# Kernel optimization log

Measured on AMD Instinct MI355X. Metric: run time of the kernel, lower is better.

The kernel has to match this reference:

```python
import jax, jax.numpy as jnp
import numpy as np

HIDDEN = 512
ANN = 512


def setup_inputs() -> dict:
    key = jax.random.key(0)
    k1, k2, k3, k4, k5, k6 = jax.random.split(key, 6)
    B, S = 32, 4096
    prev_hidden_state = jax.random.normal(k1, (B, HIDDEN), dtype=jnp.float32)
    annotations = jax.random.normal(k2, (B, S, ANN), dtype=jnp.float32)
    in_dim = HIDDEN + ANN
    # Kaiming-uniform-ish init like torch Linear
    lim1 = 1.0 / np.sqrt(in_dim)
    W1 = jax.random.uniform(k3, (in_dim, HIDDEN), dtype=jnp.float32, minval=-lim1, maxval=lim1)
    b1 = jax.random.uniform(k4, (HIDDEN,), dtype=jnp.float32, minval=-lim1, maxval=lim1)
    lim2 = 1.0 / np.sqrt(HIDDEN)
    W2 = jax.random.uniform(k5, (HIDDEN, 1), dtype=jnp.float32, minval=-lim2, maxval=lim2)
    b2 = jax.random.uniform(k6, (1,), dtype=jnp.float32, minval=-lim2, maxval=lim2)
    return {"prev_hidden_state": prev_hidden_state, "annotations": annotations,
            "W1": W1, "b1": b1, "W2": W2, "b2": b2}


def reference(prev_hidden_state, annotations, W1, b1, W2, b2):
    # Split W1 so we never materialize the [B,S,hidden+ann] concat:
    # concat([h_rep, ann]) @ W1 == h @ W1[:H] + ann @ W1[H:]
    W1_h, W1_a = W1[:HIDDEN], W1[HIDDEN:]
    # [B,1,H] + [B,S,H] -> [B,S,H]
    pre = prev_hidden_state @ W1_h  # [B,H]
    hidden = jnp.tanh(pre[:, None, :] + jnp.einsum('bsa,ah->bsh', annotations, W1_a) + b1)
    score = jnp.einsum('bsh,h->bs', hidden, W2[:, 0]) + b2[0]  # [B,S]
    alpha = jax.nn.softmax(score, axis=1)  # legacy F.softmax default dim=1
    # alpha.bmm(annotations): [B,1,S] @ [B,S,A] -> [B,1,A]
    context = jnp.einsum('bs,bsa->ba', alpha, annotations)[:, None, :]
    return context
```

## Files before the change

kernel.cpp:

```cpp
#include <hip/hip_runtime.h>

#define HID 512
#define SEQ 4096
#define NB 32
#define BS 64
#define NSB 8
#define CPB 8
#define CH2 1026

typedef __attribute__((ext_vector_type(8))) __bf16 bf16x8;
typedef __attribute__((ext_vector_type(16))) float f32x16;

__device__ __forceinline__ float tanh_fast(float v) {
    float e = __expf(2.f * v);
    return 1.f - __fdividef(2.f, e + 1.f);
}

__global__ void build_w1af(const float* __restrict__ W1,
                           unsigned short* __restrict__ w1af) {
    __shared__ float tile[64][65];
    int t = threadIdx.x;
    int lane = t & 63;
    int r4 = t >> 6;
    int k0 = blockIdx.x * 64;
    int h0 = blockIdx.y * 64;
#pragma unroll
    for (int i = 0; i < 16; ++i) {
        int r = i * 4 + r4;
        tile[r][lane] = W1[(size_t)(HID + k0 + r) * HID + h0 + lane];
    }
    __syncthreads();
#pragma unroll
    for (int i = 0; i < 16; ++i) {
        int hr = i * 4 + r4;
        int h = h0 + hr, k = k0 + lane;
        __bf16 bv = (__bf16)tile[lane][hr];
        int ht = h >> 5, hl = h & 31;
        int ks = k >> 4, g = (k >> 3) & 1, j = k & 7;
        size_t off = (((size_t)ht * 32 + ks) * 64 + g * 32 + hl) * 8 + j;
        w1af[off] = *(unsigned short*)&bv;
    }
}

__global__ void pre_partial(const float* __restrict__ prev,
                            const float* __restrict__ W1,
                            float* __restrict__ pre_part) {
    __shared__ float pl[128];
    int kc = blockIdx.x;
    int b  = blockIdx.y;
    int t  = threadIdx.x;
    if (t < 128) pl[t] = prev[b * HID + kc * 128 + t];
    __syncthreads();
    int h0 = 2 * t;
    float ax = 0.f, ay = 0.f;
    for (int k = 0; k < 128; ++k) {
        float pv = pl[k];
        float2 wv = *(const float2*)(W1 + (size_t)(kc * 128 + k) * HID + h0);
        ax += pv * wv.x;
        ay += pv * wv.y;
    }
    float* dst = pre_part + ((size_t)b * 4 + kc) * HID + h0;
    dst[0] = ax; dst[1] = ay;
}

__global__ __launch_bounds__(1024, 4)
void score_ctx(const float* __restrict__ ann,
               const unsigned short* __restrict__ w1af,
               const float* __restrict__ pre_part,
               const float* __restrict__ b1,
               const float* __restrict__ W2,
               float* __restrict__ cout) {
    __shared__ unsigned short annA[BS * 512];
    __shared__ unsigned short annB[BS * 512];
    __shared__ float pre_lds[512];
    __shared__ float w2_lds[512];
    __shared__ float red[16][64];
    __shared__ float p_lds[64];
    __shared__ float md[2];

    const int sb = blockIdx.x, b = blockIdx.y;
    const int t = threadIdx.x;
    const int wv = t >> 6;
    const int lane = t & 63;
    const int sl = lane & 31;
    const int g = lane >> 5;

    if (t < 512) {
        float pp = b1[t];
#pragma unroll
        for (int kc = 0; kc < 4; ++kc)
            pp += pre_part[((size_t)b * 4 + kc) * HID + t];
        pre_lds[t] = pp;
    } else {
        w2_lds[t - 512] = W2[t - 512];
    }

    const float* abase = ann + ((size_t)b * SEQ + (size_t)sb * (CPB * BS)) * 512;

    float4 sf[8];
    {
#pragma unroll
        for (int i = 0; i < 4; ++i) {
            int idx = t + i * 1024;
            const float4* src = (const float4*)(abase + (size_t)(idx >> 6) * 512 + (idx & 63) * 8);
            sf[2 * i] = src[0]; sf[2 * i + 1] = src[1];
        }
#pragma unroll
        for (int i = 0; i < 4; ++i) {
            int idx = t + i * 1024;
            int row = idx >> 6, k8 = (idx & 63) * 8;
            bf16x8 pk;
            pk[0] = (__bf16)sf[2*i].x;   pk[1] = (__bf16)sf[2*i].y;
            pk[2] = (__bf16)sf[2*i].z;   pk[3] = (__bf16)sf[2*i].w;
            pk[4] = (__bf16)sf[2*i+1].x; pk[5] = (__bf16)sf[2*i+1].y;
            pk[6] = (__bf16)sf[2*i+1].z; pk[7] = (__bf16)sf[2*i+1].w;
            unsigned boff = ((unsigned)(row * 512 + k8) * 2u) ^ ((unsigned)(row & 7) << 4);
            *(bf16x8*)((char*)annA + boff) = pk;
        }
    }
    __syncthreads();

    float m_run = -3.0e38f, d_run = 0.f, ctx = 0.f;
    const int col = t & 511, half = t >> 9;

    const unsigned short* wb = w1af + (size_t)wv * 16384 + (size_t)lane * 8;
    const unsigned be0 = (unsigned)(sl * 512 + g * 8) * 2u;
    const unsigned be1 = (unsigned)((32 + sl) * 512 + g * 8) * 2u;
    const unsigned swz = (unsigned)(sl & 7) << 4;

#pragma unroll 1
    for (int c = 0; c < CPB; ++c) {
        unsigned short* curb = (c & 1) ? annB : annA;
        unsigned short* nxtb = (c & 1) ? annA : annB;

        if (c < CPB - 1) {
            const float* ab = abase + (size_t)(c + 1) * BS * 512;
#pragma unroll
            for (int i = 0; i < 4; ++i) {
                int idx = t + i * 1024;
                const float4* src = (const float4*)(ab + (size_t)(idx >> 6) * 512 + (idx & 63) * 8);
                sf[2 * i] = src[0]; sf[2 * i + 1] = src[1];
            }
        }

        f32x16 acc0, acc1;
#pragma unroll
        for (int r = 0; r < 16; ++r) { acc0[r] = 0.f; acc1[r] = 0.f; }
#pragma unroll 2
        for (int ks = 0; ks < 32; ++ks) {
            bf16x8 a = *(const bf16x8*)(wb + ks * 512);
            bf16x8 bf0 = *(const bf16x8*)((const char*)curb + ((be0 + (unsigned)ks * 32u) ^ swz));
            bf16x8 bf1 = *(const bf16x8*)((const char*)curb + ((be1 + (unsigned)ks * 32u) ^ swz));
            acc0 = __builtin_amdgcn_mfma_f32_32x32x16_bf16(a, bf0, acc0, 0, 0, 0);
            acc1 = __builtin_amdgcn_mfma_f32_32x32x16_bf16(a, bf1, acc1, 0, 0, 0);
        }

        float sp0 = 0.f, sp1 = 0.f;
#pragma unroll
        for (int r = 0; r < 16; ++r) {
            int h = wv * 32 + (r & 3) + 8 * (r >> 2) + 4 * g;
            float pr = pre_lds[h], w2v = w2_lds[h];
            sp0 += w2v * tanh_fast(acc0[r] + pr);
            sp1 += w2v * tanh_fast(acc1[r] + pr);
        }
        sp0 += __shfl_xor(sp0, 32);
        sp1 += __shfl_xor(sp1, 32);
        if (lane < 32) { red[wv][lane] = sp0; red[wv][32 + lane] = sp1; }
        __syncthreads();

        if (wv == 0) {
            float sc = 0.f;
#pragma unroll
            for (int q = 0; q < 16; ++q) sc += red[q][lane];
            float m = sc;
#pragma unroll
            for (int off = 32; off; off >>= 1) m = fmaxf(m, __shfl_xor(m, off));
            float p = __expf(sc - m);
            float d = p;
#pragma unroll
            for (int off = 32; off; off >>= 1) d += __shfl_xor(d, off);
            p_lds[lane] = p;
            if (lane == 0) { md[0] = m; md[1] = d; }
        }
        __syncthreads();

        float m_c = md[0], d_c = md[1];
        float m_new = fmaxf(m_run, m_c);
        float sc_old = __expf(m_run - m_new);
        float sc_c = __expf(m_c - m_new);
        d_run = d_run * sc_old + d_c * sc_c;
        float na = 0.f;
        const char* cb8 = (const char*)curb;
#pragma unroll 8
        for (int s2 = 0; s2 < 32; ++s2) {
            int s = half * 32 + s2;
            unsigned boff = ((unsigned)(s * 512 + col) * 2u) ^ ((unsigned)(s & 7) << 4);
            unsigned short us = *(const unsigned short*)(cb8 + boff);
            na += p_lds[s] * __uint_as_float((unsigned)us << 16);
        }
        ctx = ctx * sc_old + na * sc_c;
        m_run = m_new;

        if (c < CPB - 1) {
            __syncthreads();
#pragma unroll
            for (int i = 0; i < 4; ++i) {
                int idx = t + i * 1024;
                int row = idx >> 6, k8 = (idx & 63) * 8;
                bf16x8 pk;
                pk[0] = (__bf16)sf[2*i].x;   pk[1] = (__bf16)sf[2*i].y;
                pk[2] = (__bf16)sf[2*i].z;   pk[3] = (__bf16)sf[2*i].w;
                pk[4] = (__bf16)sf[2*i+1].x; pk[5] = (__bf16)sf[2*i+1].y;
                pk[6] = (__bf16)sf[2*i+1].z; pk[7] = (__bf16)sf[2*i+1].w;
                unsigned boff = ((unsigned)(row * 512 + k8) * 2u) ^ ((unsigned)(row & 7) << 4);
                *(bf16x8*)((char*)nxtb + boff) = pk;
            }
            __syncthreads();
        }
    }

    float* cb = cout + ((size_t)b * NSB + sb) * CH2;
    cb[2 + half * 512 + col] = ctx;
    if (t == 0) { cb[0] = m_run; cb[1] = d_run; }
}

__global__ void finalize_ctx(const float* __restrict__ cout,
                             float* __restrict__ out) {
    int b = blockIdx.x, t = threadIdx.x;
    float ms[NSB];
    float M = -3.0e38f;
#pragma unroll
    for (int s = 0; s < NSB; ++s) {
        ms[s] = cout[((size_t)b * NSB + s) * CH2];
        M = fmaxf(M, ms[s]);
    }
    float D = 0.f, val = 0.f;
#pragma unroll
    for (int s = 0; s < NSB; ++s) {
        const float* cb = cout + ((size_t)b * NSB + s) * CH2;
        float e = __expf(ms[s] - M);
        D += e * cb[1];
        val += e * (cb[2 + t] + cb[2 + 512 + t]);
    }
    out[(size_t)b * 512 + t] = val / D;
}

extern "C" void kernel_launch(void* const* d_in, const int* in_sizes, int n_in,
                              void* d_out, int out_size, void* d_ws, size_t ws_size,
                              hipStream_t stream) {
    (void)in_sizes; (void)n_in; (void)out_size; (void)ws_size;
    const float* prev = (const float*)d_in[0];
    const float* ann  = (const float*)d_in[1];
    const float* W1   = (const float*)d_in[2];
    const float* b1   = (const float*)d_in[3];
    const float* W2   = (const float*)d_in[4];
    float* out = (float*)d_out;

    char* ws = (char*)d_ws;
    unsigned short* w1af = (unsigned short*)ws;
    float* pre_part = (float*)(ws + 524288);
    float* cout     = (float*)(ws + 524288 + 262144);

    build_w1af<<<dim3(8, 8), dim3(256), 0, stream>>>(W1, w1af);
    pre_partial<<<dim3(4, NB), dim3(256), 0, stream>>>(prev, W1, pre_part);
    score_ctx<<<dim3(NSB, NB), dim3(1024), 0, stream>>>(ann, w1af, pre_part, b1, W2, cout);
    finalize_ctx<<<dim3(NB), dim3(512), 0, stream>>>(cout, out);
}
```

Measured before the change: 151.6 us.

## Use 128-row chunks with 512 threads and 2x4 MFMA register tiles per wave

Chunk size doubles to 128 rows and the block shrinks to 8 waves. Each wave now computes a 64x128 output tile with eight MFMA accumulators, so each W1 fragment is reused across four B tiles. The double-buffered LDS with register prefetch is replaced by a single buffer that is loaded synchronously, which removes the overlap of global loads with compute. The context accumulation reads two bf16 values per 32-bit LDS load.

```diff
diff --git a/kernel.cpp b/kernel.cpp
--- a/kernel.cpp
+++ b/kernel.cpp
@@ -3,9 +3,9 @@
 #define HID 512
 #define SEQ 4096
 #define NB 32
-#define BS 64
+#define BS 128
 #define NSB 8
-#define CPB 8
+#define CPB 4
 #define CH2 1026
 
 typedef __attribute__((ext_vector_type(8))) __bf16 bf16x8;
@@ -63,19 +63,18 @@
     dst[0] = ax; dst[1] = ay;
 }
 
-__global__ __launch_bounds__(1024, 4)
+__global__ __launch_bounds__(512, 2)
 void score_ctx(const float* __restrict__ ann,
                const unsigned short* __restrict__ w1af,
                const float* __restrict__ pre_part,
                const float* __restrict__ b1,
                const float* __restrict__ W2,
                float* __restrict__ cout) {
-    __shared__ unsigned short annA[BS * 512];
-    __shared__ unsigned short annB[BS * 512];
+    __shared__ unsigned short ann_lds[BS * 512];
     __shared__ float pre_lds[512];
     __shared__ float w2_lds[512];
-    __shared__ float red[16][64];
-    __shared__ float p_lds[64];
+    __shared__ float red[8][BS];
+    __shared__ float p_lds[BS];
     __shared__ float md[2];
 
     const int sb = blockIdx.x, b = blockIdx.y;
@@ -85,142 +84,134 @@
     const int sl = lane & 31;
     const int g = lane >> 5;
 
-    if (t < 512) {
+    {
         float pp = b1[t];
 #pragma unroll
         for (int kc = 0; kc < 4; ++kc)
             pp += pre_part[((size_t)b * 4 + kc) * HID + t];
         pre_lds[t] = pp;
-    } else {
-        w2_lds[t - 512] = W2[t - 512];
-    }
-
-    const float* abase = ann + ((size_t)b * SEQ + (size_t)sb * (CPB * BS)) * 512;
-
-    float4 sf[8];
-    {
-#pragma unroll
-        for (int i = 0; i < 4; ++i) {
-            int idx = t + i * 1024;
-            const float4* src = (const float4*)(abase + (size_t)(idx >> 6) * 512 + (idx & 63) * 8);
-            sf[2 * i] = src[0]; sf[2 * i + 1] = src[1];
-        }
-#pragma unroll
-        for (int i = 0; i < 4; ++i) {
-            int idx = t + i * 1024;
-            int row = idx >> 6, k8 = (idx & 63) * 8;
-            bf16x8 pk;
-            pk[0] = (__bf16)sf[2*i].x;   pk[1] = (__bf16)sf[2*i].y;
-            pk[2] = (__bf16)sf[2*i].z;   pk[3] = (__bf16)sf[2*i].w;
-            pk[4] = (__bf16)sf[2*i+1].x; pk[5] = (__bf16)sf[2*i+1].y;
-            pk[6] = (__bf16)sf[2*i+1].z; pk[7] = (__bf16)sf[2*i+1].w;
-            unsigned boff = ((unsigned)(row * 512 + k8) * 2u) ^ ((unsigned)(row & 7) << 4);
-            *(bf16x8*)((char*)annA + boff) = pk;
-        }
-    }
-    __syncthreads();
-
-    float m_run = -3.0e38f, d_run = 0.f, ctx = 0.f;
-    const int col = t & 511, half = t >> 9;
-
-    const unsigned short* wb = w1af + (size_t)wv * 16384 + (size_t)lane * 8;
-    const unsigned be0 = (unsigned)(sl * 512 + g * 8) * 2u;
-    const unsigned be1 = (unsigned)((32 + sl) * 512 + g * 8) * 2u;
+        w2_lds[t] = W2[t];
+    }
+
+    const float* abase0 = ann + ((size_t)b * SEQ + (size_t)sb * (CPB * BS)) * 512;
+
+    float m_run = -3.0e38f, d_run = 0.f;
+    float ctxa = 0.f, ctxb = 0.f;
+    const int cp = (t & 255) * 2;
+    const int h2 = t >> 8;
+
+    const unsigned short* wb0 = w1af + (size_t)(2 * wv) * 16384 + (size_t)lane * 8;
+    const unsigned short* wb1 = wb0 + 16384;
     const unsigned swz = (unsigned)(sl & 7) << 4;
+    const unsigned rb0 = (unsigned)(( 0 + sl) * 1024 + g * 16);
+    const unsigned rb1 = (unsigned)((32 + sl) * 1024 + g * 16);
+    const unsigned rb2 = (unsigned)((64 + sl) * 1024 + g * 16);
+    const unsigned rb3 = (unsigned)((96 + sl) * 1024 + g * 16);
 
 #pragma unroll 1
     for (int c = 0; c < CPB; ++c) {
-        unsigned short* curb = (c & 1) ? annB : annA;
-        unsigned short* nxtb = (c & 1) ? annA : annB;
-
-        if (c < CPB - 1) {
-            const float* ab = abase + (size_t)(c + 1) * BS * 512;
-#pragma unroll
-            for (int i = 0; i < 4; ++i) {
-                int idx = t + i * 1024;
-                const float4* src = (const float4*)(ab + (size_t)(idx >> 6) * 512 + (idx & 63) * 8);
-                sf[2 * i] = src[0]; sf[2 * i + 1] = src[1];
-            }
-        }
-
-        f32x16 acc0, acc1;
-#pragma unroll
-        for (int r = 0; r < 16; ++r) { acc0[r] = 0.f; acc1[r] = 0.f; }
+        __syncthreads();
+
+        const float* ab = abase0 + (size_t)c * BS * 512;
+#pragma unroll 4
+        for (int i = 0; i < 16; ++i) {
+            int idx = t + i * 512;
+            int row = idx >> 6, k8 = (idx & 63) * 8;
+            const float4* src = (const float4*)(ab + (size_t)row * 512 + k8);
+            float4 f0 = src[0], f1 = src[1];
+            bf16x8 pk;
+            pk[0] = (__bf16)f0.x; pk[1] = (__bf16)f0.y;
+            pk[2] = (__bf16)f0.z; pk[3] = (__bf16)f0.w;
+            pk[4] = (__bf16)f1.x; pk[5] = (__bf16)f1.y;
+            pk[6] = (__bf16)f1.z; pk[7] = (__bf16)f1.w;
+            unsigned boff = ((unsigned)(row * 512 + k8) * 2u) ^ ((unsigned)(row & 7) << 4);
+            *(bf16x8*)((char*)ann_lds + boff) = pk;
+        }
+        __syncthreads();
+
+        f32x16 a00, a01, a02, a03, a10, a11, a12, a13;
+#pragma unroll
+        for (int r = 0; r < 16; ++r) {
+            a00[r] = 0.f; a01[r] = 0.f; a02[r] = 0.f; a03[r] = 0.f;
+            a10[r] = 0.f; a11[r] = 0.f; a12[r] = 0.f; a13[r] = 0.f;
+        }
 #pragma unroll 2
         for (int ks = 0; ks < 32; ++ks) {
-            bf16x8 a = *(const bf16x8*)(wb + ks * 512);
-            bf16x8 bf0 = *(const bf16x8*)((const char*)curb + ((be0 + (unsigned)ks * 32u) ^ swz));
-            bf16x8 bf1 = *(const bf16x8*)((const char*)curb + ((be1 + (unsigned)ks * 32u) ^ swz));
-            acc0 = __builtin_amdgcn_mfma_f32_32x32x16_bf16(a, bf0, acc0, 0, 0, 0);
-            acc1 = __builtin_amdgcn_mfma_f32_32x32x16_bf16(a, bf1, acc1, 0, 0, 0);
-        }
-
-        float sp0 = 0.f, sp1 = 0.f;
+            bf16x8 A0 = *(const bf16x8*)(wb0 + ks * 512);
+            bf16x8 A1 = *(const bf16x8*)(wb1 + ks * 512);
+            unsigned kb = (unsigned)ks * 32u;
+            bf16x8 B0 = *(const bf16x8*)((const char*)ann_lds + ((rb0 + kb) ^ swz));
+            bf16x8 B1 = *(const bf16x8*)((const char*)ann_lds + ((rb1 + kb) ^ swz));
+            bf16x8 B2 = *(const bf16x8*)((const char*)ann_lds + ((rb2 + kb) ^ swz));
+            bf16x8 B3 = *(const bf16x8*)((const char*)ann_lds + ((rb3 + kb) ^ swz));
+            a00 = __builtin_amdgcn_mfma_f32_32x32x16_bf16(A0, B0, a00, 0, 0, 0);
+            a10 = __builtin_amdgcn_mfma_f32_32x32x16_bf16(A1, B0, a10, 0, 0, 0);
+            a01 = __builtin_amdgcn_mfma_f32_32x32x16_bf16(A0, B1, a01, 0, 0, 0);
+            a11 = __builtin_amdgcn_mfma_f32_32x32x16_bf16(A1, B1, a11, 0, 0, 0);
+            a02 = __builtin_amdgcn_mfma_f32_32x32x16_bf16(A0, B2, a02, 0, 0, 0);
+            a12 = __builtin_amdgcn_mfma_f32_32x32x16_bf16(A1, B2, a12, 0, 0, 0);
+            a03 = __builtin_amdgcn_mfma_f32_32x32x16_bf16(A0, B3, a03, 0, 0, 0);
+            a13 = __builtin_amdgcn_mfma_f32_32x32x16_bf16(A1, B3, a13, 0, 0, 0);
+        }
+
+        float sp0 = 0.f, sp1 = 0.f, sp2 = 0.f, sp3 = 0.f;
 #pragma unroll
         for (int r = 0; r < 16; ++r) {
-            int h = wv * 32 + (r & 3) + 8 * (r >> 2) + 4 * g;
-            float pr = pre_lds[h], w2v = w2_lds[h];
-            sp0 += w2v * tanh_fast(acc0[r] + pr);
-            sp1 += w2v * tanh_fast(acc1[r] + pr);
-        }
-        sp0 += __shfl_xor(sp0, 32);
-        sp1 += __shfl_xor(sp1, 32);
-        if (lane < 32) { red[wv][lane] = sp0; red[wv][32 + lane] = sp1; }
+            int hl = (r & 3) + 8 * (r >> 2) + 4 * g;
+            int ha = wv * 64 + hl, hb = wv * 64 + 32 + hl;
+            float pa = pre_lds[ha], wa = w2_lds[ha];
+            float pb = pre_lds[hb], wbv = w2_lds[hb];
+            sp0 += wa * tanh_fast(a00[r] + pa) + wbv * tanh_fast(a10[r] + pb);
+            sp1 += wa * tanh_fast(a01[r] + pa) + wbv * tanh_fast(a11[r] + pb);
+            sp2 += wa * tanh_fast(a02[r] + pa) + wbv * tanh_fast(a12[r] + pb);
+            sp3 += wa * tanh_fast(a03[r] + pa) + wbv * tanh_fast(a13[r] + pb);
+        }
+        sp0 += __shfl_xor(sp0, 32); sp1 += __shfl_xor(sp1, 32);
+        sp2 += __shfl_xor(sp2, 32); sp3 += __shfl_xor(sp3, 32);
+        if (lane < 32) {
+            red[wv][ 0 + lane] = sp0; red[wv][32 + lane] = sp1;
+            red[wv][64 + lane] = sp2; red[wv][96 + lane] = sp3;
+        }
         __syncthreads();
 
         if (wv == 0) {
-            float sc = 0.f;
-#pragma unroll
-            for (int q = 0; q < 16; ++q) sc += red[q][lane];
-            float m = sc;
+            float sa = 0.f, sb2 = 0.f;
+#pragma unroll
+            for (int q = 0; q < 8; ++q) { sa += red[q][lane]; sb2 += red[q][64 + lane]; }
+            float m = fmaxf(sa, sb2);
 #pragma unroll
             for (int off = 32; off; off >>= 1) m = fmaxf(m, __shfl_xor(m, off));
-            float p = __expf(sc - m);
-            float d = p;
+            float pa = __expf(sa - m), pb = __expf(sb2 - m);
+            float d = pa + pb;
 #pragma unroll
             for (int off = 32; off; off >>= 1) d += __shfl_xor(d, off);
-            p_lds[lane] = p;
+            p_lds[lane] = pa; p_lds[64 + lane] = pb;
             if (lane == 0) { md[0] = m; md[1] = d; }
         }
         __syncthreads();
 
         float m_c = md[0], d_c = md[1];
         float m_new = fmaxf(m_run, m_c);
-        float sc_old = __expf(m_run - m_new);
-        float sc_c = __expf(m_c - m_new);
-        d_run = d_run * sc_old + d_c * sc_c;
-        float na = 0.f;
-        const char* cb8 = (const char*)curb;
+        float so = __expf(m_run - m_new), sc = __expf(m_c - m_new);
+        d_run = d_run * so + d_c * sc;
+        float na = 0.f, nb = 0.f;
 #pragma unroll 8
-        for (int s2 = 0; s2 < 32; ++s2) {
-            int s = half * 32 + s2;
-            unsigned boff = ((unsigned)(s * 512 + col) * 2u) ^ ((unsigned)(s & 7) << 4);
-            unsigned short us = *(const unsigned short*)(cb8 + boff);
-            na += p_lds[s] * __uint_as_float((unsigned)us << 16);
-        }
-        ctx = ctx * sc_old + na * sc_c;
+        for (int s2 = 0; s2 < 64; ++s2) {
+            int s = h2 * 64 + s2;
+            unsigned boff = ((unsigned)(s * 1024 + cp * 2)) ^ ((unsigned)(s & 7) << 4);
+            unsigned u = *(const unsigned*)((const char*)ann_lds + boff);
+            float p = p_lds[s];
+            na += p * __uint_as_float(u << 16);
+            nb += p * __uint_as_float(u & 0xFFFF0000u);
+        }
+        ctxa = ctxa * so + na * sc;
+        ctxb = ctxb * so + nb * sc;
         m_run = m_new;
-
-        if (c < CPB - 1) {
-            __syncthreads();
-#pragma unroll
-            for (int i = 0; i < 4; ++i) {
-                int idx = t + i * 1024;
-                int row = idx >> 6, k8 = (idx & 63) * 8;
-                bf16x8 pk;
-                pk[0] = (__bf16)sf[2*i].x;   pk[1] = (__bf16)sf[2*i].y;
-                pk[2] = (__bf16)sf[2*i].z;   pk[3] = (__bf16)sf[2*i].w;
-                pk[4] = (__bf16)sf[2*i+1].x; pk[5] = (__bf16)sf[2*i+1].y;
-                pk[6] = (__bf16)sf[2*i+1].z; pk[7] = (__bf16)sf[2*i+1].w;
-                unsigned boff = ((unsigned)(row * 512 + k8) * 2u) ^ ((unsigned)(row & 7) << 4);
-                *(bf16x8*)((char*)nxtb + boff) = pk;
-            }
-            __syncthreads();
-        }
     }
 
     float* cb = cout + ((size_t)b * NSB + sb) * CH2;
-    cb[2 + half * 512 + col] = ctx;
+    cb[2 + h2 * 512 + cp]     = ctxa;
+    cb[2 + h2 * 512 + cp + 1] = ctxb;
     if (t == 0) { cb[0] = m_run; cb[1] = d_run; }
 }
 
@@ -263,6 +254,6 @@
 
     build_w1af<<<dim3(8, 8), dim3(256), 0, stream>>>(W1, w1af);
     pre_partial<<<dim3(4, NB), dim3(256), 0, stream>>>(prev, W1, pre_part);
-    score_ctx<<<dim3(NSB, NB), dim3(1024), 0, stream>>>(ann, w1af, pre_part, b1, W2, cout);
+    score_ctx<<<dim3(NSB, NB), dim3(512), 0, stream>>>(ann, w1af, pre_part, b1, W2, cout);
     finalize_ctx<<<dim3(NB), dim3(512), 0, stream>>>(cout, out);
 }
```

Result: faster. 142.5 us (-6.0%).

## Halve score_ctx block to 512 threads with 2x2 MFMA tiles per wave

Applied to the files above, without the earlier changes.

Shrinks the score/context block from 1024 to 512 threads. Each wave now computes a 64x64 output tile with four 32x32 MFMA accumulators, reusing each A and B fragment twice. The per-chunk softmax is done redundantly in every wave using shuffles instead of a wave-0 pass through LDS, which removes one barrier per chunk. Annotation loads become nontemporal float4 loads, and each thread produces one context column, which halves the partial-output size. The trade-off is more registers per thread (16 prefetch vectors and 4 accumulators) and fewer threads to hide the global-load latency.

```diff
diff --git a/kernel.cpp b/kernel.cpp
--- a/kernel.cpp
+++ b/kernel.cpp
@@ -6,10 +6,12 @@
 #define BS 64
 #define NSB 8
 #define CPB 8
-#define CH2 1026
+#define CH 514
 
 typedef __attribute__((ext_vector_type(8))) __bf16 bf16x8;
+typedef __attribute__((ext_vector_type(4))) __bf16 bf16x4;
 typedef __attribute__((ext_vector_type(16))) float f32x16;
+typedef __attribute__((ext_vector_type(4))) float f32x4;
 
 __device__ __forceinline__ float tanh_fast(float v) {
     float e = __expf(2.f * v);
@@ -63,20 +65,18 @@
     dst[0] = ax; dst[1] = ay;
 }
 
-__global__ __launch_bounds__(1024, 4)
+__global__ __launch_bounds__(512, 2)
 void score_ctx(const float* __restrict__ ann,
                const unsigned short* __restrict__ w1af,
                const float* __restrict__ pre_part,
                const float* __restrict__ b1,
                const float* __restrict__ W2,
                float* __restrict__ cout) {
-    __shared__ unsigned short annA[BS * 512];
-    __shared__ unsigned short annB[BS * 512];
+    __shared__ unsigned short bufA[BS * 512];
+    __shared__ unsigned short bufB[BS * 512];
     __shared__ float pre_lds[512];
     __shared__ float w2_lds[512];
-    __shared__ float red[16][64];
-    __shared__ float p_lds[64];
-    __shared__ float md[2];
+    __shared__ float red[8][64];
 
     const int sb = blockIdx.x, b = blockIdx.y;
     const int t = threadIdx.x;
@@ -85,142 +85,135 @@
     const int sl = lane & 31;
     const int g = lane >> 5;
 
-    if (t < 512) {
+    {
         float pp = b1[t];
 #pragma unroll
         for (int kc = 0; kc < 4; ++kc)
             pp += pre_part[((size_t)b * 4 + kc) * HID + t];
         pre_lds[t] = pp;
-    } else {
-        w2_lds[t - 512] = W2[t - 512];
-    }
-
-    const float* abase = ann + ((size_t)b * SEQ + (size_t)sb * (CPB * BS)) * 512;
-
-    float4 sf[8];
+        w2_lds[t] = W2[t];
+    }
+
+    const float* abase0 = ann + ((size_t)b * SEQ + (size_t)sb * (CPB * BS)) * 512;
+
+    f32x4 sf[16];
+
     {
-#pragma unroll
-        for (int i = 0; i < 4; ++i) {
-            int idx = t + i * 1024;
-            const float4* src = (const float4*)(abase + (size_t)(idx >> 6) * 512 + (idx & 63) * 8);
-            sf[2 * i] = src[0]; sf[2 * i + 1] = src[1];
-        }
-#pragma unroll
-        for (int i = 0; i < 4; ++i) {
-            int idx = t + i * 1024;
-            int row = idx >> 6, k8 = (idx & 63) * 8;
-            bf16x8 pk;
-            pk[0] = (__bf16)sf[2*i].x;   pk[1] = (__bf16)sf[2*i].y;
-            pk[2] = (__bf16)sf[2*i].z;   pk[3] = (__bf16)sf[2*i].w;
-            pk[4] = (__bf16)sf[2*i+1].x; pk[5] = (__bf16)sf[2*i+1].y;
-            pk[6] = (__bf16)sf[2*i+1].z; pk[7] = (__bf16)sf[2*i+1].w;
-            unsigned boff = ((unsigned)(row * 512 + k8) * 2u) ^ ((unsigned)(row & 7) << 4);
-            *(bf16x8*)((char*)annA + boff) = pk;
+        const float* ab = abase0;
+#pragma unroll
+        for (int i = 0; i < 16; ++i) {
+            int idx = t + i * 512;
+            sf[i] = __builtin_nontemporal_load((const f32x4*)(ab) + idx);
+        }
+#pragma unroll
+        for (int i = 0; i < 16; ++i) {
+            int idx = t + i * 512;
+            int row = idx >> 7, c4 = idx & 127;
+            bf16x4 pk;
+            pk[0] = (__bf16)sf[i][0]; pk[1] = (__bf16)sf[i][1];
+            pk[2] = (__bf16)sf[i][2]; pk[3] = (__bf16)sf[i][3];
+            unsigned boff = ((unsigned)(row * 1024 + c4 * 8)) ^ ((unsigned)(row & 7) << 4);
+            *(bf16x4*)((char*)bufA + boff) = pk;
         }
     }
     __syncthreads();
 
     float m_run = -3.0e38f, d_run = 0.f, ctx = 0.f;
-    const int col = t & 511, half = t >> 9;
-
-    const unsigned short* wb = w1af + (size_t)wv * 16384 + (size_t)lane * 8;
-    const unsigned be0 = (unsigned)(sl * 512 + g * 8) * 2u;
-    const unsigned be1 = (unsigned)((32 + sl) * 512 + g * 8) * 2u;
+
+    const unsigned short* wb0 = w1af + (size_t)(2 * wv) * 16384 + (size_t)lane * 8;
+    const unsigned short* wb1 = wb0 + 16384;
     const unsigned swz = (unsigned)(sl & 7) << 4;
+    const unsigned rb0 = (unsigned)(( 0 + sl) * 1024 + g * 16);
+    const unsigned rb1 = (unsigned)((32 + sl) * 1024 + g * 16);
 
 #pragma unroll 1
     for (int c = 0; c < CPB; ++c) {
-        unsigned short* curb = (c & 1) ? annB : annA;
-        unsigned short* nxtb = (c & 1) ? annA : annB;
+        unsigned short* cur = (c & 1) ? bufB : bufA;
+        unsigned short* nxt = (c & 1) ? bufA : bufB;
 
         if (c < CPB - 1) {
-            const float* ab = abase + (size_t)(c + 1) * BS * 512;
-#pragma unroll
-            for (int i = 0; i < 4; ++i) {
-                int idx = t + i * 1024;
-                const float4* src = (const float4*)(ab + (size_t)(idx >> 6) * 512 + (idx & 63) * 8);
-                sf[2 * i] = src[0]; sf[2 * i + 1] = src[1];
+            const float* ab = abase0 + (size_t)(c + 1) * BS * 512;
+#pragma unroll
+            for (int i = 0; i < 16; ++i) {
+                int idx = t + i * 512;
+                sf[i] = __builtin_nontemporal_load((const f32x4*)(ab) + idx);
             }
         }
 
-        f32x16 acc0, acc1;
-#pragma unroll
-        for (int r = 0; r < 16; ++r) { acc0[r] = 0.f; acc1[r] = 0.f; }
-#pragma unroll 2
+        f32x16 acc00, acc01, acc10, acc11;
+#pragma unroll
+        for (int r = 0; r < 16; ++r) { acc00[r] = 0.f; acc01[r] = 0.f; acc10[r] = 0.f; acc11[r] = 0.f; }
+#pragma unroll
         for (int ks = 0; ks < 32; ++ks) {
-            bf16x8 a = *(const bf16x8*)(wb + ks * 512);
-            bf16x8 bf0 = *(const bf16x8*)((const char*)curb + ((be0 + (unsigned)ks * 32u) ^ swz));
-            bf16x8 bf1 = *(const bf16x8*)((const char*)curb + ((be1 + (unsigned)ks * 32u) ^ swz));
-            acc0 = __builtin_amdgcn_mfma_f32_32x32x16_bf16(a, bf0, acc0, 0, 0, 0);
-            acc1 = __builtin_amdgcn_mfma_f32_32x32x16_bf16(a, bf1, acc1, 0, 0, 0);
+            bf16x8 A0 = *(const bf16x8*)(wb0 + ks * 512);
+            bf16x8 A1 = *(const bf16x8*)(wb1 + ks * 512);
+            unsigned kb = (unsigned)ks * 32u;
+            bf16x8 B0 = *(const bf16x8*)((const char*)cur + ((rb0 + kb) ^ swz));
+            bf16x8 B1 = *(const bf16x8*)((const char*)cur + ((rb1 + kb) ^ swz));
+            acc00 = __builtin_amdgcn_mfma_f32_32x32x16_bf16(A0, B0, acc00, 0, 0, 0);
+            acc10 = __builtin_amdgcn_mfma_f32_32x32x16_bf16(A1, B0, acc10, 0, 0, 0);
+            acc01 = __builtin_amdgcn_mfma_f32_32x32x16_bf16(A0, B1, acc01, 0, 0, 0);
+            acc11 = __builtin_amdgcn_mfma_f32_32x32x16_bf16(A1, B1, acc11, 0, 0, 0);
         }
 
         float sp0 = 0.f, sp1 = 0.f;
 #pragma unroll
         for (int r = 0; r < 16; ++r) {
-            int h = wv * 32 + (r & 3) + 8 * (r >> 2) + 4 * g;
-            float pr = pre_lds[h], w2v = w2_lds[h];
-            sp0 += w2v * tanh_fast(acc0[r] + pr);
-            sp1 += w2v * tanh_fast(acc1[r] + pr);
+            int hl = (r & 3) + 8 * (r >> 2) + 4 * g;
+            int ha = wv * 64 + hl, hb = ha + 32;
+            float pa = pre_lds[ha], wa = w2_lds[ha];
+            float pb = pre_lds[hb], wb = w2_lds[hb];
+            sp0 += wa * tanh_fast(acc00[r] + pa) + wb * tanh_fast(acc10[r] + pb);
+            sp1 += wa * tanh_fast(acc01[r] + pa) + wb * tanh_fast(acc11[r] + pb);
         }
         sp0 += __shfl_xor(sp0, 32);
         sp1 += __shfl_xor(sp1, 32);
-        if (lane < 32) { red[wv][lane] = sp0; red[wv][32 + lane] = sp1; }
+        if (lane < 32) { red[wv][sl] = sp0; red[wv][32 + sl] = sp1; }
         __syncthreads();
 
-        if (wv == 0) {
-            float sc = 0.f;
-#pragma unroll
-            for (int q = 0; q < 16; ++q) sc += red[q][lane];
-            float m = sc;
-#pragma unroll
-            for (int off = 32; off; off >>= 1) m = fmaxf(m, __shfl_xor(m, off));
-            float p = __expf(sc - m);
-            float d = p;
-#pragma unroll
-            for (int off = 32; off; off >>= 1) d += __shfl_xor(d, off);
-            p_lds[lane] = p;
-            if (lane == 0) { md[0] = m; md[1] = d; }
+        float sc = 0.f;
+#pragma unroll
+        for (int q = 0; q < 8; ++q) sc += red[q][lane];
+        float m = sc;
+#pragma unroll
+        for (int off = 32; off; off >>= 1) m = fmaxf(m, __shfl_xor(m, off));
+        float p = __expf(sc - m);
+        float d = p;
+#pragma unroll
+        for (int off = 32; off; off >>= 1) d += __shfl_xor(d, off);
+
+        float m_new = fmaxf(m_run, m);
+        float so = __expf(m_run - m_new), s_c = __expf(m - m_new);
+        d_run = d_run * so + d * s_c;
+
+        float na = 0.f;
+#pragma unroll 8
+        for (int s = 0; s < BS; ++s) {
+            float ps = __shfl(p, s);
+            unsigned boff = ((unsigned)(s * 1024 + t * 2)) ^ ((unsigned)(s & 7) << 4);
+            unsigned short us = *(const unsigned short*)((const char*)cur + boff);
+            na += ps * __uint_as_float((unsigned)us << 16);
+        }
+        ctx = ctx * so + na * s_c;
+        m_run = m_new;
+
+        if (c < CPB - 1) {
+#pragma unroll
+            for (int i = 0; i < 16; ++i) {
+                int idx = t + i * 512;
+                int row = idx >> 7, c4 = idx & 127;
+                bf16x4 pk;
+                pk[0] = (__bf16)sf[i][0]; pk[1] = (__bf16)sf[i][1];
+                pk[2] = (__bf16)sf[i][2]; pk[3] = (__bf16)sf[i][3];
+                unsigned boff = ((unsigned)(row * 1024 + c4 * 8)) ^ ((unsigned)(row & 7) << 4);
+                *(bf16x4*)((char*)nxt + boff) = pk;
+            }
         }
         __syncthreads();
-
-        float m_c = md[0], d_c = md[1];
-        float m_new = fmaxf(m_run, m_c);
-        float sc_old = __expf(m_run - m_new);
-        float sc_c = __expf(m_c - m_new);
-        d_run = d_run * sc_old + d_c * sc_c;
-        float na = 0.f;
-        const char* cb8 = (const char*)curb;
-#pragma unroll 8
-        for (int s2 = 0; s2 < 32; ++s2) {
-            int s = half * 32 + s2;
-            unsigned boff = ((unsigned)(s * 512 + col) * 2u) ^ ((unsigned)(s & 7) << 4);
-            unsigned short us = *(const unsigned short*)(cb8 + boff);
-            na += p_lds[s] * __uint_as_float((unsigned)us << 16);
-        }
-        ctx = ctx * sc_old + na * sc_c;
-        m_run = m_new;
-
-        if (c < CPB - 1) {
-            __syncthreads();
-#pragma unroll
-            for (int i = 0; i < 4; ++i) {
-                int idx = t + i * 1024;
-                int row = idx >> 6, k8 = (idx & 63) * 8;
-                bf16x8 pk;
-                pk[0] = (__bf16)sf[2*i].x;   pk[1] = (__bf16)sf[2*i].y;
-                pk[2] = (__bf16)sf[2*i].z;   pk[3] = (__bf16)sf[2*i].w;
-                pk[4] = (__bf16)sf[2*i+1].x; pk[5] = (__bf16)sf[2*i+1].y;
-                pk[6] = (__bf16)sf[2*i+1].z; pk[7] = (__bf16)sf[2*i+1].w;
-                unsigned boff = ((unsigned)(row * 512 + k8) * 2u) ^ ((unsigned)(row & 7) << 4);
-                *(bf16x8*)((char*)nxtb + boff) = pk;
-            }
-            __syncthreads();
-        }
-    }
-
-    float* cb = cout + ((size_t)b * NSB + sb) * CH2;
-    cb[2 + half * 512 + col] = ctx;
+    }
+
+    float* cb = cout + ((size_t)b * NSB + sb) * CH;
+    cb[2 + t] = ctx;
     if (t == 0) { cb[0] = m_run; cb[1] = d_run; }
 }
 
@@ -231,16 +224,16 @@
     float M = -3.0e38f;
 #pragma unroll
     for (int s = 0; s < NSB; ++s) {
-        ms[s] = cout[((size_t)b * NSB + s) * CH2];
+        ms[s] = cout[((size_t)b * NSB + s) * CH];
         M = fmaxf(M, ms[s]);
     }
     float D = 0.f, val = 0.f;
 #pragma unroll
     for (int s = 0; s < NSB; ++s) {
-        const float* cb = cout + ((size_t)b * NSB + s) * CH2;
+        const float* cb = cout + ((size_t)b * NSB + s) * CH;
         float e = __expf(ms[s] - M);
         D += e * cb[1];
-        val += e * (cb[2 + t] + cb[2 + 512 + t]);
+        val += e * cb[2 + t];
     }
     out[(size_t)b * 512 + t] = val / D;
 }
@@ -263,6 +256,6 @@
 
     build_w1af<<<dim3(8, 8), dim3(256), 0, stream>>>(W1, w1af);
     pre_partial<<<dim3(4, NB), dim3(256), 0, stream>>>(prev, W1, pre_part);
-    score_ctx<<<dim3(NSB, NB), dim3(1024), 0, stream>>>(ann, w1af, pre_part, b1, W2, cout);
+    score_ctx<<<dim3(NSB, NB), dim3(512), 0, stream>>>(ann, w1af, pre_part, b1, W2, cout);
     finalize_ctx<<<dim3(NB), dim3(512), 0, stream>>>(cout, out);
 }
```

Measured after the change: 406.5 us. 168% more time.
